# Kernel optimization log

Measured on AMD Instinct MI355X. Metric: run time of the kernel, lower is better.

The kernel has to match this reference:

```python
import jax, jax.numpy as jnp
import numpy as np

CUTOFF = 5.0
BOX = 15.0
SPECIES = [1, 6, 8]
N_NODES = 10000
N_EDGES = 200000
ETAS = [0.01, 0.05, 0.1]
ZETAS = [1.0, 2.0, 4.0, 8.0]
LAMBDAS = [-1.0, 1.0]


def _cartesian_params():
    # matches torch.cartesian_prod(etas, zetas, lambdas): etas outermost
    e, zt, lb = np.meshgrid(np.float32(ETAS), np.float32(ZETAS), np.float32(LAMBDAS), indexing='ij')
    return e.ravel(), zt.ravel(), lb.ravel()  # each [24]


def _build_triplets(rng):
    # edges: edge_index[0]=j (source), edge_index[1]=i (target)
    j = rng.integers(0, N_NODES, N_EDGES)
    i = rng.integers(0, N_NODES, N_EDGES)
    edge_shift = rng.integers(-1, 2, (N_EDGES, 3)).astype(np.float32)
    # CSR of adj_t (row=i, col=j): for edge e, triplet partners k are cols of row j[e]
    order = np.argsort(i, kind='stable')
    cols = j[order]
    cnt = np.bincount(i, minlength=N_NODES)
    rowptr = np.concatenate([[0], np.cumsum(cnt)])
    num_trip = cnt[j]
    T = int(num_trip.sum())
    e_of_t = np.repeat(np.arange(N_EDGES), num_trip)
    starts = np.repeat(np.cumsum(num_trip) - num_trip, num_trip)
    local = np.arange(T) - starts
    idx_k = cols[rowptr[j[e_of_t]] + local]
    idx_i = i[e_of_t]
    idx_j = j[e_of_t]
    shift_t = edge_shift[e_of_t]
    m = idx_i != idx_k
    return idx_i[m], idx_j[m], idx_k[m], shift_t[m]


def setup_inputs() -> dict:
    rng = np.random.default_rng(0)
    pos = rng.uniform(0.0, BOX, (N_NODES, 3)).astype(np.float32)
    cell = (np.eye(3, dtype=np.float32) * BOX)[None]  # [1,3,3]
    z = np.asarray(SPECIES, dtype=np.int64)[rng.integers(0, 3, N_NODES)]
    batch = np.zeros(N_NODES, dtype=np.int64)
    idx_i, idx_j, idx_k, edge_shift_i = _build_triplets(rng)
    etas, zetas, lambdas = _cartesian_params()
    return {
        'pos': jnp.asarray(pos), 'cell': jnp.asarray(cell),
        'z': jnp.asarray(z), 'batch': jnp.asarray(batch),
        'idx_i': jnp.asarray(idx_i), 'idx_j': jnp.asarray(idx_j), 'idx_k': jnp.asarray(idx_k),
        'edge_shift_i': jnp.asarray(edge_shift_i),
        'etas': jnp.asarray(etas), 'zetas': jnp.asarray(zetas), 'lambdas': jnp.asarray(lambdas),
    }


def _cutoff_fn(r):
    return 0.5 * (jnp.cos(jnp.pi * r / CUTOFF) + 1.0) * (r < CUTOFF).astype(r.dtype)


def reference(pos, cell, z, batch, idx_i, idx_j, idx_k, edge_shift_i, etas, zetas, lambdas):
    n_nodes = pos.shape[0]
    pos_i = pos[idx_i]                       # [T,3]
    cell_t = cell[batch[idx_i]]              # [T,3,3]
    shift = jnp.einsum('ni,nij->nj', edge_shift_i, cell_t)
    vec_ij = pos[idx_j] - pos_i + shift
    vec_ik = pos[idx_k] - pos_i + shift
    r_ij = jnp.linalg.norm(vec_ij, axis=-1)
    r_ik = jnp.linalg.norm(vec_ik, axis=-1)
    r_jk = jnp.linalg.norm(vec_ik - vec_ij, axis=-1)
    cos_ijk = jnp.sum(vec_ij * vec_ik, axis=-1) / (r_ij * r_ik + 1e-12)

    # [P,T] angular descriptor; base (1 + lambda*cos) >= 0 since lambda = +/-1
    G4 = (jnp.power(2.0, 1.0 - zetas)[:, None]
          * jnp.power(1.0 + lambdas[:, None] * cos_ijk[None, :], zetas[:, None])
          * jnp.exp(-etas[:, None] * (r_ij**2 + r_ik**2 + r_jk**2)[None, :] / CUTOFF**2)
          * (_cutoff_fn(r_ij) * _cutoff_fn(r_ik) * _cutoff_fn(r_jk))[None, :])

    zj = z[idx_j]
    zk = z[idx_k]
    outs = []
    for sp in SPECIES:
        mask = ((zj == sp) & (zk == sp)).astype(G4.dtype)
        outs.append(jax.ops.segment_sum((G4 * mask).T, idx_i, num_segments=n_nodes).T / 2)
    pairs = [(SPECIES[a], SPECIES[b]) for a in range(len(SPECIES)) for b in range(a + 1, len(SPECIES))]
    for sp_j, sp_k in pairs:
        mask = (((zj == sp_j) & (zk == sp_k)) | ((zj == sp_k) & (zk == sp_j))).astype(G4.dtype)
        outs.append(jax.ops.segment_sum((G4 * mask).T, idx_i, num_segments=n_nodes).T / 2)
    return jnp.concatenate(outs, axis=0)  # [6*P, N]
```

## Files before the change

### kernel.cpp

```cpp
#include <hip/hip_runtime.h>
#include <math.h>

#define CUTOFF_R  5.0f
#define CUT2      25.0f
#define INV_CUT2  (1.0f / 25.0f)
#define PI_OVER_CUT (3.14159265358979323846f / CUTOFF_R)
#define NPARAM 24
#define NATOMS 10000

__device__ __noinline__ void rare_accumulate(
    int i, int j, int k,
    float vjx, float vjy, float vjz,
    float vkx, float vky, float vkz,
    float r2ij, float r2ik, float r2jk,
    const int* __restrict__ z,
    const float* __restrict__ etas,
    float* __restrict__ out, int N)
{
    float rij = sqrtf(r2ij);
    float rik = sqrtf(r2ik);
    float rjk = sqrtf(r2jk);

    float fc = 0.125f * (cosf(PI_OVER_CUT * rij) + 1.0f)
                      * (cosf(PI_OVER_CUT * rik) + 1.0f)
                      * (cosf(PI_OVER_CUT * rjk) + 1.0f);

    float cos_ijk = (vjx * vkx + vjy * vky + vjz * vkz) / (rij * rik + 1e-12f);
    float ssum = (r2ij + r2ik + r2jk) * INV_CUT2;

    int zj = z[j], zk = z[k];
    int a = (zj == 1) ? 0 : ((zj == 6) ? 1 : 2);
    int c = (zk == 1) ? 0 : ((zk == 6) ? 1 : 2);
    int ch = (a == c) ? a : (2 + a + c);

    float* obase = out + (size_t)ch * NPARAM * N + i;
    float fch = 0.5f * fc;

    float bm = 1.0f - cos_ijk;
    float bp = 1.0f + cos_ijk;
    float pw[4][2];
    pw[0][0] = bm;                 pw[0][1] = bp;
    pw[1][0] = bm * bm;            pw[1][1] = bp * bp;
    pw[2][0] = pw[1][0]*pw[1][0];  pw[2][1] = pw[1][1]*pw[1][1];
    pw[3][0] = pw[2][0]*pw[2][0];  pw[3][1] = pw[2][1]*pw[2][1];
    const float coef[4] = {1.0f, 0.5f, 0.125f, 0.0078125f};

    #pragma unroll
    for (int e = 0; e < 3; ++e) {
        float ee = expf(-etas[e * 8] * ssum) * fch;
        #pragma unroll
        for (int zi = 0; zi < 4; ++zi) {
            float cz = coef[zi] * ee;
            atomicAdd(obase + (size_t)(e * 8 + zi * 2 + 0) * N, cz * pw[zi][0]);
            atomicAdd(obase + (size_t)(e * 8 + zi * 2 + 1) * N, cz * pw[zi][1]);
        }
    }
}

__global__ __launch_bounds__(1024, 1) void g4_kernel(
    const float* __restrict__ pos,
    const float* __restrict__ cell,
    const int*   __restrict__ z,
    const int*   __restrict__ idx_i,
    const int*   __restrict__ idx_j,
    const int*   __restrict__ idx_k,
    const float* __restrict__ shift,
    const float* __restrict__ etas,
    float* __restrict__ out,
    int T, int N)
{
    __shared__ float spos[3 * NATOMS];
    {
        const float4* pos4  = reinterpret_cast<const float4*>(pos);
        float4*       spos4 = reinterpret_cast<float4*>(spos);
        const int nvec = (3 * NATOMS) / 4;
        for (int u = threadIdx.x; u < nvec; u += blockDim.x)
            spos4[u] = pos4[u];
    }
    __syncthreads();

    float C00 = cell[0], C01 = cell[1], C02 = cell[2];
    float C10 = cell[3], C11 = cell[4], C12 = cell[5];
    float C20 = cell[6], C21 = cell[7], C22 = cell[8];

    const int nQuads   = (T + 3) >> 2;
    const int gstride  = gridDim.x * blockDim.x;

    for (int q = blockIdx.x * blockDim.x + threadIdx.x; q < nQuads; q += gstride) {
        int base = q * 4;
        if (base + 4 <= T) {
            int4 vi = *reinterpret_cast<const int4*>(idx_i + base);
            int4 vj = *reinterpret_cast<const int4*>(idx_j + base);
            int4 vk = *reinterpret_cast<const int4*>(idx_k + base);
            int ii[4] = {vi.x, vi.y, vi.z, vi.w};
            int jj[4] = {vj.x, vj.y, vj.z, vj.w};
            int kk[4] = {vk.x, vk.y, vk.z, vk.w};
            float sf[12];
            {
                const float4* sp = reinterpret_cast<const float4*>(shift + 3 * base);
                float4 a = sp[0], b = sp[1], c = sp[2];
                sf[0]=a.x; sf[1]=a.y; sf[2]=a.z;  sf[3]=a.w;
                sf[4]=b.x; sf[5]=b.y; sf[6]=b.z;  sf[7]=b.w;
                sf[8]=c.x; sf[9]=c.y; sf[10]=c.z; sf[11]=c.w;
            }

            #pragma unroll
            for (int m = 0; m < 4; ++m) {
                int i = ii[m], j = jj[m], k = kk[m];
                float s0 = sf[3*m], s1 = sf[3*m+1], s2 = sf[3*m+2];
                float shx = s0 * C00 + s1 * C10 + s2 * C20;
                float shy = s0 * C01 + s1 * C11 + s2 * C21;
                float shz = s0 * C02 + s1 * C12 + s2 * C22;

                float pix = spos[3*i+0], piy = spos[3*i+1], piz = spos[3*i+2];
                float vjx = spos[3*j+0] - pix + shx;
                float vjy = spos[3*j+1] - piy + shy;
                float vjz = spos[3*j+2] - piz + shz;
                float vkx = spos[3*k+0] - pix + shx;
                float vky = spos[3*k+1] - piy + shy;
                float vkz = spos[3*k+2] - piz + shz;

                float r2ij = vjx*vjx + vjy*vjy + vjz*vjz;
                float r2ik = vkx*vkx + vky*vky + vkz*vkz;
                float dx = vkx - vjx, dy = vky - vjy, dz = vkz - vjz;
                float r2jk = dx*dx + dy*dy + dz*dz;

                if ((r2ij < CUT2) & (r2ik < CUT2) & (r2jk < CUT2)) {
                    rare_accumulate(i, j, k, vjx, vjy, vjz, vkx, vky, vkz,
                                    r2ij, r2ik, r2jk, z, etas, out, N);
                }
            }
        } else {
            for (int m = 0; m < 4; ++m) {
                int t = base + m;
                if (t >= T) break;
                int i = idx_i[t], j = idx_j[t], k = idx_k[t];
                float s0 = shift[3*t], s1 = shift[3*t+1], s2 = shift[3*t+2];
                float shx = s0 * C00 + s1 * C10 + s2 * C20;
                float shy = s0 * C01 + s1 * C11 + s2 * C21;
                float shz = s0 * C02 + s1 * C12 + s2 * C22;
                float pix = spos[3*i+0], piy = spos[3*i+1], piz = spos[3*i+2];
                float vjx = spos[3*j+0] - pix + shx;
                float vjy = spos[3*j+1] - piy + shy;
                float vjz = spos[3*j+2] - piz + shz;
                float vkx = spos[3*k+0] - pix + shx;
                float vky = spos[3*k+1] - piy + shy;
                float vkz = spos[3*k+2] - piz + shz;
                float r2ij = vjx*vjx + vjy*vjy + vjz*vjz;
                float r2ik = vkx*vkx + vky*vky + vkz*vkz;
                float dx = vkx - vjx, dy = vky - vjy, dz = vkz - vjz;
                float r2jk = dx*dx + dy*dy + dz*dz;
                if ((r2ij < CUT2) & (r2ik < CUT2) & (r2jk < CUT2)) {
                    rare_accumulate(i, j, k, vjx, vjy, vjz, vkx, vky, vkz,
                                    r2ij, r2ik, r2jk, z, etas, out, N);
                }
            }
        }
    }
}

extern "C" void kernel_launch(void* const* d_in, const int* in_sizes, int n_in,
                              void* d_out, int out_size, void* d_ws, size_t ws_size,
                              hipStream_t stream) {
    const float* pos     = (const float*)d_in[0];
    const float* cell    = (const float*)d_in[1];
    const int*   z       = (const int*)d_in[2];
    const int*   idx_i   = (const int*)d_in[4];
    const int*   idx_j   = (const int*)d_in[5];
    const int*   idx_k   = (const int*)d_in[6];
    const float* shift   = (const float*)d_in[7];
    const float* etas    = (const float*)d_in[8];
    float* out = (float*)d_out;

    int T = in_sizes[4];
    int N = in_sizes[0] / 3;

    hipMemsetAsync(d_out, 0, (size_t)out_size * sizeof(float), stream);

    int block = 1024;
    int grid  = 256;
    g4_kernel<<<grid, block, 0, stream>>>(pos, cell, z,
                                          idx_i, idx_j, idx_k, shift,
                                          etas, out, T, N);
}
```

Before: 146.7 us.

## Pad positions to float4 in LDS and give each thread 16 triplets

Stores atom positions in shared memory as padded float4 so each atom's position is fetched with one vector LDS read instead of three scalar reads. Swaps the grid-stride loop over quads for a one-shot mapping with 16 triplets per thread, sizing the grid from T, and drops the occupancy hint from launch bounds. More blocks now each reload the whole position table into shared memory (160KB as float4), so staging traffic grows, and the larger LDS footprint limits how many blocks fit per CU.

```diff
diff --git a/kernel.cpp b/kernel.cpp
--- a/kernel.cpp
+++ b/kernel.cpp
@@ -7,6 +7,7 @@
 #define PI_OVER_CUT (3.14159265358979323846f / CUTOFF_R)
 #define NPARAM 24
 #define NATOMS 10000
+#define TPT 16
 
 __device__ __noinline__ void rare_accumulate(
     int i, int j, int k,
@@ -57,7 +58,7 @@
     }
 }
 
-__global__ __launch_bounds__(1024, 1) void g4_kernel(
+__global__ __launch_bounds__(1024) void g4_kernel(
     const float* __restrict__ pos,
     const float* __restrict__ cell,
     const int*   __restrict__ z,
@@ -69,13 +70,9 @@
     float* __restrict__ out,
     int T, int N)
 {
-    __shared__ float spos[3 * NATOMS];
-    {
-        const float4* pos4  = reinterpret_cast<const float4*>(pos);
-        float4*       spos4 = reinterpret_cast<float4*>(spos);
-        const int nvec = (3 * NATOMS) / 4;
-        for (int u = threadIdx.x; u < nvec; u += blockDim.x)
-            spos4[u] = pos4[u];
+    __shared__ float4 spos[NATOMS];
+    for (int u = threadIdx.x; u < NATOMS; u += blockDim.x) {
+        spos[u] = make_float4(pos[3*u], pos[3*u+1], pos[3*u+2], 0.0f);
     }
     __syncthreads();
 
@@ -83,77 +80,82 @@
     float C10 = cell[3], C11 = cell[4], C12 = cell[5];
     float C20 = cell[6], C21 = cell[7], C22 = cell[8];
 
-    const int nQuads   = (T + 3) >> 2;
-    const int gstride  = gridDim.x * blockDim.x;
+    int tid  = blockIdx.x * blockDim.x + threadIdx.x;
+    int base = tid * TPT;
+    if (base >= T) return;
 
-    for (int q = blockIdx.x * blockDim.x + threadIdx.x; q < nQuads; q += gstride) {
-        int base = q * 4;
-        if (base + 4 <= T) {
-            int4 vi = *reinterpret_cast<const int4*>(idx_i + base);
-            int4 vj = *reinterpret_cast<const int4*>(idx_j + base);
-            int4 vk = *reinterpret_cast<const int4*>(idx_k + base);
-            int ii[4] = {vi.x, vi.y, vi.z, vi.w};
-            int jj[4] = {vj.x, vj.y, vj.z, vj.w};
-            int kk[4] = {vk.x, vk.y, vk.z, vk.w};
-            float sf[12];
-            {
-                const float4* sp = reinterpret_cast<const float4*>(shift + 3 * base);
-                float4 a = sp[0], b = sp[1], c = sp[2];
-                sf[0]=a.x; sf[1]=a.y; sf[2]=a.z;  sf[3]=a.w;
-                sf[4]=b.x; sf[5]=b.y; sf[6]=b.z;  sf[7]=b.w;
-                sf[8]=c.x; sf[9]=c.y; sf[10]=c.z; sf[11]=c.w;
+    if (base + TPT <= T) {
+        int ii[TPT], jj[TPT], kk[TPT];
+        float ss[3 * TPT];
+        #pragma unroll
+        for (int q = 0; q < TPT / 4; ++q) {
+            int4 a = *reinterpret_cast<const int4*>(idx_i + base + 4 * q);
+            int4 b = *reinterpret_cast<const int4*>(idx_j + base + 4 * q);
+            int4 c = *reinterpret_cast<const int4*>(idx_k + base + 4 * q);
+            ii[4*q+0]=a.x; ii[4*q+1]=a.y; ii[4*q+2]=a.z; ii[4*q+3]=a.w;
+            jj[4*q+0]=b.x; jj[4*q+1]=b.y; jj[4*q+2]=b.z; jj[4*q+3]=b.w;
+            kk[4*q+0]=c.x; kk[4*q+1]=c.y; kk[4*q+2]=c.z; kk[4*q+3]=c.w;
+        }
+        #pragma unroll
+        for (int q = 0; q < (3 * TPT) / 4; ++q) {
+            float4 s = *reinterpret_cast<const float4*>(shift + 3 * base + 4 * q);
+            ss[4*q+0]=s.x; ss[4*q+1]=s.y; ss[4*q+2]=s.z; ss[4*q+3]=s.w;
+        }
+
+        #pragma unroll
+        for (int m = 0; m < TPT; ++m) {
+            int i = ii[m], j = jj[m], k = kk[m];
+            float s0 = ss[3*m], s1 = ss[3*m+1], s2 = ss[3*m+2];
+            float shx = s0 * C00 + s1 * C10 + s2 * C20;
+            float shy = s0 * C01 + s1 * C11 + s2 * C21;
+            float shz = s0 * C02 + s1 * C12 + s2 * C22;
+
+            float4 pi = spos[i];
+            float4 pj = spos[j];
+            float4 pk = spos[k];
+
+            float vjx = pj.x - pi.x + shx;
+            float vjy = pj.y - pi.y + shy;
+            float vjz = pj.z - pi.z + shz;
+            float vkx = pk.x - pi.x + shx;
+            float vky = pk.y - pi.y + shy;
+            float vkz = pk.z - pi.z + shz;
+
+            float r2ij = vjx*vjx + vjy*vjy + vjz*vjz;
+            float r2ik = vkx*vkx + vky*vky + vkz*vkz;
+            float dx = vkx - vjx, dy = vky - vjy, dz = vkz - vjz;
+            float r2jk = dx*dx + dy*dy + dz*dz;
+
+            if ((r2ij < CUT2) & (r2ik < CUT2) & (r2jk < CUT2)) {
+                rare_accumulate(i, j, k, vjx, vjy, vjz, vkx, vky, vkz,
+                                r2ij, r2ik, r2jk, z, etas, out, N);
             }
-
-            #pragma unroll
-            for (int m = 0; m < 4; ++m) {
-                int i = ii[m], j = jj[m], k = kk[m];
-                float s0 = sf[3*m], s1 = sf[3*m+1], s2 = sf[3*m+2];
-                float shx = s0 * C00 + s1 * C10 + s2 * C20;
-                float shy = s0 * C01 + s1 * C11 + s2 * C21;
-                float shz = s0 * C02 + s1 * C12 + s2 * C22;
-
-                float pix = spos[3*i+0], piy = spos[3*i+1], piz = spos[3*i+2];
-                float vjx = spos[3*j+0] - pix + shx;
-                float vjy = spos[3*j+1] - piy + shy;
-                float vjz = spos[3*j+2] - piz + shz;
-                float vkx = spos[3*k+0] - pix + shx;
-                float vky = spos[3*k+1] - piy + shy;
-                float vkz = spos[3*k+2] - piz + shz;
-
-                float r2ij = vjx*vjx + vjy*vjy + vjz*vjz;
-                float r2ik = vkx*vkx + vky*vky + vkz*vkz;
-                float dx = vkx - vjx, dy = vky - vjy, dz = vkz - vjz;
-                float r2jk = dx*dx + dy*dy + dz*dz;
-
-                if ((r2ij < CUT2) & (r2ik < CUT2) & (r2jk < CUT2)) {
-                    rare_accumulate(i, j, k, vjx, vjy, vjz, vkx, vky, vkz,
-                                    r2ij, r2ik, r2jk, z, etas, out, N);
-                }
-            }
-        } else {
-            for (int m = 0; m < 4; ++m) {
-                int t = base + m;
-                if (t >= T) break;
-                int i = idx_i[t], j = idx_j[t], k = idx_k[t];
-                float s0 = shift[3*t], s1 = shift[3*t+1], s2 = shift[3*t+2];
-                float shx = s0 * C00 + s1 * C10 + s2 * C20;
-                float shy = s0 * C01 + s1 * C11 + s2 * C21;
-                float shz = s0 * C02 + s1 * C12 + s2 * C22;
-                float pix = spos[3*i+0], piy = spos[3*i+1], piz = spos[3*i+2];
-                float vjx = spos[3*j+0] - pix + shx;
-                float vjy = spos[3*j+1] - piy + shy;
-                float vjz = spos[3*j+2] - piz + shz;
-                float vkx = spos[3*k+0] - pix + shx;
-                float vky = spos[3*k+1] - piy + shy;
-                float vkz = spos[3*k+2] - piz + shz;
-                float r2ij = vjx*vjx + vjy*vjy + vjz*vjz;
-                float r2ik = vkx*vkx + vky*vky + vkz*vkz;
-                float dx = vkx - vjx, dy = vky - vjy, dz = vkz - vjz;
-                float r2jk = dx*dx + dy*dy + dz*dz;
-                if ((r2ij < CUT2) & (r2ik < CUT2) & (r2jk < CUT2)) {
-                    rare_accumulate(i, j, k, vjx, vjy, vjz, vkx, vky, vkz,
-                                    r2ij, r2ik, r2jk, z, etas, out, N);
-                }
+        }
+    } else {
+        for (int m = 0; m < TPT; ++m) {
+            int t = base + m;
+            if (t >= T) break;
+            int i = idx_i[t], j = idx_j[t], k = idx_k[t];
+            float s0 = shift[3*t], s1 = shift[3*t+1], s2 = shift[3*t+2];
+            float shx = s0 * C00 + s1 * C10 + s2 * C20;
+            float shy = s0 * C01 + s1 * C11 + s2 * C21;
+            float shz = s0 * C02 + s1 * C12 + s2 * C22;
+            float4 pi = spos[i];
+            float4 pj = spos[j];
+            float4 pk = spos[k];
+            float vjx = pj.x - pi.x + shx;
+            float vjy = pj.y - pi.y + shy;
+            float vjz = pj.z - pi.z + shz;
+            float vkx = pk.x - pi.x + shx;
+            float vky = pk.y - pi.y + shy;
+            float vkz = pk.z - pi.z + shz;
+            float r2ij = vjx*vjx + vjy*vjy + vjz*vjz;
+            float r2ik = vkx*vkx + vky*vky + vkz*vkz;
+            float dx = vkx - vjx, dy = vky - vjy, dz = vkz - vjz;
+            float r2jk = dx*dx + dy*dy + dz*dz;
+            if ((r2ij < CUT2) & (r2ik < CUT2) & (r2jk < CUT2)) {
+                rare_accumulate(i, j, k, vjx, vjy, vjz, vkx, vky, vkz,
+                                r2ij, r2ik, r2jk, z, etas, out, N);
             }
         }
     }
@@ -178,7 +180,8 @@
     hipMemsetAsync(d_out, 0, (size_t)out_size * sizeof(float), stream);
 
     int block = 1024;
-    int grid  = 256;
+    long long threads_needed = ((long long)T + TPT - 1) / TPT;
+    int grid = (int)((threads_needed + block - 1) / block);
     g4_kernel<<<grid, block, 0, stream>>>(pos, cell, z,
                                           idx_i, idx_j, idx_k, shift,
                                           etas, out, T, N);
```

Result: slower. 173.0 us (+17.9%).
